# Kernel tuning notes

Hardware: AMD Instinct MI355X
Metric: run time of the kernel (lower is better)

## Reference

```python
import jax, jax.numpy as jnp
import numpy as np

B, T, E, A, S, H = 1024, 64, 1024, 10, 30, 200  # batch, time, embed, actdim, stoch, deter==hidden
MIN_STD = 0.1


def _xavier(key, fan_in, fan_out):
    lim = float(np.sqrt(6.0 / (fan_in + fan_out)))
    return jax.random.uniform(key, (fan_in, fan_out), jnp.float32, -lim, lim)


def setup_inputs() -> dict:
    key = jax.random.key(0)
    ks = jax.random.split(key, 20)
    gl = 1.0 / float(np.sqrt(H))  # torch GRUCell default init bound
    inp = {
        'embed': jax.random.normal(ks[0], (B, T, E), jnp.float32),
        'action': jax.random.normal(ks[1], (B, T, A), jnp.float32),
        'eps_post': jax.random.normal(ks[2], (T, B, S), jnp.float32),
        'eps_prior': jax.random.normal(ks[3], (T, B, S), jnp.float32),
        # Linear weights stored [in, out] (transposed vs torch) so x @ W works.
        'img1_w': _xavier(ks[4], A + S, H), 'img1_b': jnp.zeros((H,), jnp.float32),
        'gru_wi': jax.random.uniform(ks[5], (H, 3 * H), jnp.float32, -gl, gl),
        'gru_wh': jax.random.uniform(ks[6], (H, 3 * H), jnp.float32, -gl, gl),
        'gru_bi': jax.random.uniform(ks[7], (3 * H,), jnp.float32, -gl, gl),
        'gru_bh': jax.random.uniform(ks[8], (3 * H,), jnp.float32, -gl, gl),
        'img2_w': _xavier(ks[9], H, H), 'img2_b': jnp.zeros((H,), jnp.float32),
        'img3_w': _xavier(ks[10], H, 2 * S), 'img3_b': jnp.zeros((2 * S,), jnp.float32),
        'obs1_w': _xavier(ks[11], H + E, H), 'obs1_b': jnp.zeros((H,), jnp.float32),
        'obs2_w': _xavier(ks[12], H, 2 * S), 'obs2_b': jnp.zeros((2 * S,), jnp.float32),
    }
    return inp


def _observe(embed, action, eps_post, eps_prior,
             img1_w, img1_b, gru_wi, gru_wh, gru_bi, gru_bh,
             img2_w, img2_b, img3_w, img3_b, obs1_w, obs1_b, obs2_w, obs2_b):
    elu = jax.nn.elu
    embed_t = jnp.transpose(embed, (1, 0, 2))   # [T,B,E]
    action_t = jnp.transpose(action, (1, 0, 2))  # [T,B,A]

    def step(carry, xs):
        stoch, deter = carry
        a, emb, ep_q, ep_p = xs
        # img_step (prior)
        x = elu(jnp.concatenate([stoch, a], -1) @ img1_w + img1_b)
        gi = x @ gru_wi + gru_bi
        gh = deter @ gru_wh + gru_bh
        ir, iz, i_n = jnp.split(gi, 3, axis=-1)
        hr, hz, h_n = jnp.split(gh, 3, axis=-1)
        r = jax.nn.sigmoid(ir + hr)
        z = jax.nn.sigmoid(iz + hz)
        n = jnp.tanh(i_n + r * h_n)
        deter = (1.0 - z) * n + z * deter
        y = elu(deter @ img2_w + img2_b) @ img3_w + img3_b
        p_mean, p_std = jnp.split(y, 2, axis=-1)
        p_std = jax.nn.softplus(p_std) + MIN_STD
        p_stoch = p_mean + p_std * ep_p  # rsample
        # obs_step (posterior)
        o = elu(jnp.concatenate([deter, emb], -1) @ obs1_w + obs1_b) @ obs2_w + obs2_b
        q_mean, q_std = jnp.split(o, 2, axis=-1)
        q_std = jax.nn.softplus(q_std) + MIN_STD
        q_stoch = q_mean + q_std * ep_q  # rsample
        out = jnp.concatenate([q_mean, q_std, q_stoch, deter,
                               p_mean, p_std, p_stoch, deter], axis=-1)
        return (q_stoch, deter), out

    init = (jnp.zeros((B, S), embed.dtype), jnp.zeros((B, H), embed.dtype))
    _, outs = jax.lax.scan(step, init, (action_t, embed_t, eps_post, eps_prior))
    # outs: [T, B, 2*(3S+H)] -> [B, T, 580]; layout: post(mean,std,stoch,deter)|prior(mean,std,stoch,deter)
    return jnp.transpose(outs, (1, 0, 2))


def reference(embed, action, eps_post, eps_prior,
              img1_w, img1_b, gru_wi, gru_wh, gru_bi, gru_bh,
              img2_w, img2_b, img3_w, img3_b, obs1_w, obs1_b, obs2_w, obs2_b):
    return _observe(embed, action, eps_post, eps_prior,
                    img1_w, img1_b, gru_wi, gru_wh, gru_bi, gru_bh,
                    img2_w, img2_b, img3_w, img3_b, obs1_w, obs1_b, obs2_w, obs2_b)
```

## Files before the change

kernel.cpp:

```cpp
#include <hip/hip_runtime.h>

#define T_ 64

typedef __attribute__((ext_vector_type(4))) float f32x4;
typedef __attribute__((ext_vector_type(8))) short s16x8;

__device__ __forceinline__ unsigned short f2bf(float f) {
  unsigned u = __float_as_uint(f);
  u = (u + 0x7FFFu + ((u >> 16) & 1u)) >> 16;
  return (unsigned short)u;
}
__device__ __forceinline__ float bf2f(unsigned short h) {
  return __uint_as_float(((unsigned)h) << 16);
}
__device__ __forceinline__ float eluf(float x) { return x > 0.f ? x : __expf(x) - 1.f; }
__device__ __forceinline__ float sigmf(float x) { return 1.f / (1.f + __expf(-x)); }
__device__ __forceinline__ float tanh_(float x) {
  float xx = fminf(fmaxf(x, -30.f), 30.f);
  float e = __expf(-2.f * xx);
  return (1.f - e) / (1.f + e);
}
__device__ __forceinline__ float softpf(float x) {
  return x > 20.f ? x : __logf(1.f + __expf(x));
}

#define OPW1   0
#define OPWI   6656
#define OPWH   126464
#define OPO1D  246272
#define OPO2   286208
#define OPI2   298496
#define OPI3   345088
#define OWIWT  359424
#define OWHWT  364416
#define OO1DWT 369408
#define OI1WT  371072
#define OO2WT  372736
#define PK_U16 373248

#define OFF_PK  26214400
#define OFF_SWZ 26960896

__device__ void pack_mat(int idx, int stride, const float* __restrict__ W,
                         int K, int N, int KT, int NT, unsigned short* __restrict__ dst) {
  int total = KT * NT * 512;
  for (int i = idx; i < total; i += stride) {
    int j = i & 7, l = (i >> 3) & 63, rem = i >> 9;
    int kt = rem % KT, nt = rem / KT;
    int n = nt * 16 + (l & 15), k = kt * 32 + (l >> 4) * 8 + j;
    float v = (k < K && n < N) ? W[(size_t)k * N + n] : 0.f;
    dst[i] = f2bf(v);
  }
}

__device__ void pack_gate(int idx, int stride, const float* __restrict__ W,
                          unsigned short* __restrict__ dst) {
  int total = 3 * 13 * 6 * 512;
  for (int i = idx; i < total; i += stride) {
    int j = i & 7, l = (i >> 3) & 63, rem = i >> 9;
    int kt = rem % 6, rem2 = rem / 6, nt = rem2 % 13, g = rem2 / 13;
    int u = nt * 16 + (l & 15);
    int k = kt * 32 + (l >> 4) * 8 + j;
    float v = (u < 200) ? W[(size_t)k * 600 + g * 200 + u] : 0.f;
    dst[i] = f2bf(v);
  }
}

__global__ void prep_weights(const float* __restrict__ w1, const float* __restrict__ wi,
                             const float* __restrict__ wh, const float* __restrict__ i2,
                             const float* __restrict__ i3, const float* __restrict__ obs1w,
                             const float* __restrict__ o2,
                             unsigned short* __restrict__ pk,
                             unsigned short* __restrict__ swz) {
  int idx = blockIdx.x * blockDim.x + threadIdx.x;
  int stride = gridDim.x * blockDim.x;
  pack_mat(idx, stride, w1, 40, 200, 1, 13, pk + OPW1);
  pack_gate(idx, stride, wi, pk + OPWI);
  pack_gate(idx, stride, wh, pk + OPWH);
  pack_mat(idx, stride, obs1w, 200, 200, 6, 13, pk + OPO1D);
  pack_mat(idx, stride, o2, 200, 60, 6, 4, pk + OPO2);
  pack_mat(idx, stride, i2, 200, 200, 7, 13, pk + OPI2);
  pack_mat(idx, stride, i3, 200, 60, 7, 4, pk + OPI3);
  for (int i = idx; i < 4992; i += stride) {
    int j = i & 7, c = (i >> 3) % 208, g = i / 1664;
    pk[OWIWT + i] = f2bf((c < 200) ? wi[(size_t)(192 + j) * 600 + g * 200 + c] : 0.f);
    pk[OWHWT + i] = f2bf((c < 200) ? wh[(size_t)(192 + j) * 600 + g * 200 + c] : 0.f);
  }
  for (int i = idx; i < 1664; i += stride) {
    int c = i >> 3, j = i & 7;
    pk[OO1DWT + i] = f2bf((c < 200) ? obs1w[(size_t)(192 + j) * 200 + c] : 0.f);
    pk[OI1WT + i]  = f2bf((c < 200) ? w1[(size_t)(32 + j) * 200 + c] : 0.f);
  }
  for (int i = idx; i < 512; i += stride) {
    int c = i >> 3, j = i & 7;
    pk[OO2WT + i] = f2bf((c < 60) ? o2[(size_t)(192 + j) * 60 + c] : 0.f);
  }
  for (int i = idx; i < 212992; i += stride) {
    int j = i & 7, l = (i >> 3) & 63, rem = i >> 9;
    int nt = rem % 13, kc = rem / 13;
    int k = kc * 32 + ((l >> 4) * 8) + j;
    int n = nt * 16 + (l & 15);
    float v = (n < 200) ? obs1w[(size_t)(200 + k) * 200 + n] : 0.0f;
    swz[i] = f2bf(v);
  }
}

__global__ __launch_bounds__(256) void emb_gemm(const float* __restrict__ embed,
                                                const float* __restrict__ obs1b,
                                                const unsigned short* __restrict__ swz,
                                                unsigned short* __restrict__ emb_pre) {
  __shared__ __align__(16) unsigned short lds_A[64][40];
  int tid = threadIdx.x;
  int lane = tid & 63, w = tid >> 6;
  int R0 = blockIdx.x * 64;
  int tt = R0 >> 10;
  int bb = R0 & 1023;

  f32x4 acc[13];
#pragma unroll
  for (int nt = 0; nt < 13; ++nt) acc[nt] = (f32x4){0.f, 0.f, 0.f, 0.f};

  int i_row = tid >> 2, cg = tid & 3;
  const float* arow = embed + ((size_t)(bb + i_row) * 64 + tt) * 1024 + cg * 8;

  for (int kc = 0; kc < 32; ++kc) {
    __syncthreads();
    {
      const float* p = arow + kc * 32;
      f32x4 a0 = *(const f32x4*)p;
      f32x4 a1 = *(const f32x4*)(p + 4);
      unsigned short* dst = &lds_A[i_row][cg * 8];
      dst[0] = f2bf(a0[0]); dst[1] = f2bf(a0[1]); dst[2] = f2bf(a0[2]); dst[3] = f2bf(a0[3]);
      dst[4] = f2bf(a1[0]); dst[5] = f2bf(a1[1]); dst[6] = f2bf(a1[2]); dst[7] = f2bf(a1[3]);
    }
    __syncthreads();
    s16x8 af = *(const s16x8*)&lds_A[w * 16 + (lane & 15)][(lane >> 4) * 8];
    const unsigned short* bp = swz + (size_t)kc * 6656 + (size_t)lane * 8;
#pragma unroll
    for (int nt = 0; nt < 13; ++nt) {
      s16x8 bfv = *(const s16x8*)(bp + nt * 512);
      acc[nt] = __builtin_amdgcn_mfma_f32_16x16x32_bf16(af, bfv, acc[nt], 0, 0, 0);
    }
  }
  int r0 = R0 + w * 16 + ((lane >> 4) << 2);
  int c0 = lane & 15;
#pragma unroll
  for (int nt = 0; nt < 13; ++nt) {
    int n = nt * 16 + c0;
    if (n < 200) {
      float bv = obs1b[n];
#pragma unroll
      for (int rr = 0; rr < 4; ++rr)
        emb_pre[(size_t)(r0 + rr) * 200 + n] = f2bf(acc[nt][rr] + bv);
    }
  }
}

#define WAITVC(n) asm volatile("s_waitcnt vmcnt(" #n ")" ::: "memory")
#define LGKM0  asm volatile("s_waitcnt lgkmcnt(0)" ::: "memory")
#define MEMCLB asm volatile("" ::: "memory")
#define BAR()  __builtin_amdgcn_s_barrier()
#define SCHED0 __builtin_amdgcn_sched_barrier(0)
#define MFMA16(A, B, C) __builtin_amdgcn_mfma_f32_16x16x32_bf16((A), (B), (C), 0, 0, 0)

typedef __attribute__((address_space(3))) unsigned int u32_lds;
typedef const __attribute__((address_space(1))) unsigned int u32_glb;

__device__ __forceinline__ void gll16(const unsigned short* g, unsigned short* l, int lane) {
  __builtin_amdgcn_global_load_lds((u32_glb*)(g + lane * 8), (u32_lds*)l, 16, 0, 0);
}

__global__ __launch_bounds__(256, 1) void scan_v6(
    const float* __restrict__ action, const float* __restrict__ eps_post,
    const float* __restrict__ img1_b, const float* __restrict__ gru_bi,
    const float* __restrict__ gru_bh, const float* __restrict__ obs2_b,
    const unsigned short* __restrict__ pk, const unsigned short* __restrict__ emb_pre,
    float* __restrict__ out) {

  __shared__ __align__(16) unsigned short ring[4][12][512];
  __shared__ __align__(16) unsigned short l_w1[13 * 512];
  __shared__ __align__(16) unsigned short l_o2[24 * 512];
  __shared__ __align__(16) unsigned short l_wiWT[3][208][8];
  __shared__ __align__(16) unsigned short l_whWT[3][208][8];
  __shared__ __align__(16) unsigned short l_o1dWT[208][8];
  __shared__ __align__(16) unsigned short l_i1WT[208][8];
  __shared__ __align__(16) unsigned short l_o2WT[64][8];
  __shared__ __align__(16) unsigned short zblk[8];
  __shared__ __align__(16) unsigned short xoA[28][16][8];
  __shared__ __align__(16) unsigned short dA[28][16][8];
  __shared__ __align__(16) unsigned short sA[8][16][8];
  __shared__ __align__(16) float s_o[60][20];
  __shared__ __align__(16) float outbuf[16][292];
  __shared__ unsigned l_toff[4][96];

  const int tid = threadIdx.x, lane = tid & 63, w = tid >> 6;
  const int arow = lane & 15, kg = lane >> 4;
  const int b0 = blockIdx.x * 16;
  const int nug = (w == 0) ? 4 : 3;
  const int SW = nug * 24;
  unsigned short* ringw = &ring[w][0][0];

  for (int i = tid; i < 28 * 16 * 8; i += 256) { (&xoA[0][0][0])[i] = 0; (&dA[0][0][0])[i] = 0; }
  for (int i = tid; i < 8 * 16 * 8; i += 256) (&sA[0][0][0])[i] = 0;
  for (int i = tid; i < 13 * 512; i += 256) l_w1[i] = pk[OPW1 + i];
  for (int i = tid; i < 24 * 512; i += 256) l_o2[i] = pk[OPO2 + i];
  for (int i = tid; i < 4992; i += 256) (&l_wiWT[0][0][0])[i] = pk[OWIWT + i];
  for (int i = tid; i < 4992; i += 256) (&l_whWT[0][0][0])[i] = pk[OWHWT + i];
  for (int i = tid; i < 1664; i += 256) (&l_o1dWT[0][0])[i] = pk[OO1DWT + i];
  for (int i = tid; i < 1664; i += 256) (&l_i1WT[0][0])[i] = pk[OI1WT + i];
  for (int i = tid; i < 512; i += 256) (&l_o2WT[0][0])[i] = pk[OO2WT + i];
  if (tid < 8) zblk[tid] = 0;
  for (int i = tid; i < 4 * 96; i += 256) {
    int ww = i / 96, tau = i % 96;
    int iu = tau / 24, r2 = tau % 24, q = r2 / 6, kt = r2 % 6;
    int ug = ww + 4 * iu;
    unsigned off;
    if (q < 3) off = OPWI + (unsigned)((q * 13 + (ug <= 12 ? ug : 12)) * 6 + kt) * 512;
    else       off = OPWH + (unsigned)((2 * 13 + (ug <= 12 ? ug : 12)) * 6 + kt) * 512;
    l_toff[ww][tau] = off;
  }

  s16x8 wB[10][6];
#pragma unroll
  for (int s = 0; s < 10; ++s) {
    const unsigned short* base;
    if (w == 0) {
      if (s < 8) { int iu = s >> 1, g = s & 1; base = pk + OPWH + (size_t)((g * 13 + 4 * iu) * 6) * 512; }
      else if (s == 8) base = pk + OPO1D + (size_t)(12 * 6) * 512;
      else base = pk + OPO1D;
    } else {
      if (s < 6) { int iu = s >> 1, g = s & 1; base = pk + OPWH + (size_t)((g * 13 + (w + 4 * iu)) * 6) * 512; }
      else base = pk + OPO1D + (size_t)(((w - 1) + 3 * (s - 6)) * 6) * 512;
    }
#pragma unroll
    for (int kt = 0; kt < 6; ++kt)
      wB[s][kt] = *(const s16x8*)(base + (size_t)kt * 512 + lane * 8);
  }

  float bsum[4][2], bi2[4], bh2[4];
#pragma unroll
  for (int iu = 0; iu < 4; ++iu) {
    int u = (w + 4 * iu) * 16 + arow;
    bool vld = (iu < nug) && (u < 200);
    int uc = vld ? u : 0;
    float m = vld ? 1.f : 0.f;
    bsum[iu][0] = m * (gru_bi[uc] + gru_bh[uc]);
    bsum[iu][1] = m * (gru_bi[200 + uc] + gru_bh[200 + uc]);
    bi2[iu] = m * gru_bi[400 + uc];
    bh2[iu] = m * gru_bh[400 + uc];
  }
  float b1v[4];
#pragma unroll
  for (int i = 0; i < 4; ++i) {
    int nt = (i < 3) ? (w + 4 * i) : 12;
    int c = nt * 16 + arow;
    b1v[i] = (c < 200) ? img1_b[c] : 0.f;
  }
  float b5 = ((w * 16 + arow) < 60) ? obs2_b[w * 16 + arow] : 0.f;

  unsigned short e16[16];
#pragma unroll
  for (int i = 0; i < 4; ++i) {
    int nt4 = (w == 0) ? 12 : ((w - 1) + 3 * i);
    int c = nt4 * 16 + arow; int cc = (c < 200) ? c : 199;
#pragma unroll
    for (int rr = 0; rr < 4; ++rr)
      e16[i * 4 + rr] = emb_pre[((size_t)(b0 + kg * 4 + rr)) * 200 + cc];
  }
  float epsv[2];
  { int i1 = (tid + 256 < 480) ? tid + 256 : 479;
    epsv[0] = eps_post[((size_t)(b0 + tid / 30)) * 30 + tid % 30];
    epsv[1] = eps_post[((size_t)(b0 + i1 / 30)) * 30 + i1 % 30]; }
  float act0, actn;
  { int sl = (lane < 40) ? (w * 40 + lane) : (w * 40);
    act0 = action[((size_t)(b0 + sl / 10) * T_ + 0) * 10 + sl % 10];
    actn = action[((size_t)(b0 + sl / 10) * T_ + 1) * 10 + sl % 10]; }
  f32x4 dv[4];
#pragma unroll
  for (int iu = 0; iu < 4; ++iu) dv[iu] = (f32x4){0.f, 0.f, 0.f, 0.f};

  __syncthreads();
  if (lane < 40) {
    int sl = w * 40 + lane; int kk = sl % 10, r = sl / 10;
    sA[(30 + kk) >> 3][r][(30 + kk) & 7] = f2bf(act0);
  }
#pragma unroll
  for (int tt = 0; tt < 12; ++tt)
    gll16(pk + l_toff[w][tt], ringw + tt * 512, lane);
  WAITVC(0);
  __syncthreads();

  for (int t = 0; t < T_; ++t) {
    {
      s16x8 a0 = *(const s16x8*)&sA[kg][arow][0];
      s16x8 a1 = *(const s16x8*)&sA[4 + kg][arow][0];
#pragma unroll
      for (int i = 0; i < 4; ++i) {
        if (i < 3 || w == 0) {
          int nt = (i < 3) ? (w + 4 * i) : 12;
          int c = nt * 16 + arow;
          s16x8 B0 = *(const s16x8*)&l_w1[nt * 512 + lane * 8];
          f32x4 acc = {b1v[i], b1v[i], b1v[i], b1v[i]};
          acc = MFMA16(a0, B0, acc);
          s16x8 B1 = *(const s16x8*)((kg == 0) ? &l_i1WT[c][0] : &zblk[0]);
          acc = MFMA16(a1, B1, acc);
          if (c < 200) {
#pragma unroll
            for (int rr = 0; rr < 4; ++rr)
              xoA[c >> 3][kg * 4 + rr][c & 7] = f2bf(eluf(acc[rr]));
          }
        }
      }
    }
    LGKM0; BAR();

    {
#pragma unroll
      for (int iu = 0; iu < 4; ++iu) {
        if (iu < 3 || w == 0) {
          const int uu = (w + 4 * iu) * 16 + arow;
          const int uuc = (uu < 208) ? uu : 207;
          s16x8 ax[6], ad[6];
#pragma unroll
          for (int kt = 0; kt < 6; ++kt) {
            ax[kt] = *(const s16x8*)&xoA[kt * 4 + kg][arow][0];
            ad[kt] = *(const s16x8*)&dA[kt * 4 + kg][arow][0];
          }
          s16x8 ax6 = *(const s16x8*)&xoA[24 + kg][arow][0];
          s16x8 ad6 = *(const s16x8*)&dA[24 + kg][arow][0];
          f32x4 gv[2], gin, ghn;
#pragma unroll
          for (int q = 0; q < 4; ++q) {
            const int beta = iu * 4 + q;
            if (beta < 2) { WAITVC(30); } else { WAITVC(6); }
            float b = (q < 2) ? bsum[iu][q & 1] : ((q == 2) ? bi2[iu] : bh2[iu]);
            f32x4 acc = {b, b, b, b};
#pragma unroll
            for (int kt = 0; kt < 6; ++kt) {
              const int slot = (beta * 6 + kt) % 12;
              s16x8 Bv = *(const s16x8*)(ringw + slot * 512 + lane * 8);
              acc = MFMA16((q == 3) ? ad[kt] : ax[kt], Bv, acc);
            }
            MEMCLB; SCHED0;
#pragma unroll
            for (int k2 = 0; k2 < 6; ++k2) {
              const int ttc = beta * 6 + 12 + k2;
              int tm = (ttc >= SW) ? ttc - SW : ttc;
              gll16(pk + l_toff[w][tm], ringw + ((ttc % 12) * 512), lane);
            }
            if (q < 2) {
              { const unsigned short* wp = (kg == 0) ? &l_wiWT[q][uuc][0] : &zblk[0];
                acc = MFMA16(ax6, *(const s16x8*)wp, acc); }
              const int s_ = iu * 2 + q;
#pragma unroll
              for (int kt = 0; kt < 6; ++kt) acc = MFMA16(ad[kt], wB[s_][kt], acc);
              { const unsigned short* wp = (kg == 0) ? &l_whWT[q][uuc][0] : &zblk[0];
                acc = MFMA16(ad6, *(const s16x8*)wp, acc); }
              gv[q] = acc;
            } else if (q == 2) {
              const unsigned short* wp = (kg == 0) ? &l_wiWT[2][uuc][0] : &zblk[0];
              gin = MFMA16(ax6, *(const s16x8*)wp, acc);
            } else {
              const unsigned short* wp = (kg == 0) ? &l_whWT[2][uuc][0] : &zblk[0];
              ghn = MFMA16(ad6, *(const s16x8*)wp, acc);
            }
          }
#pragma unroll
          for (int rr = 0; rr < 4; ++rr) {
            float r = sigmf(gv[0][rr]);
            float z = sigmf(gv[1][rr]);
            float n = tanh_(gin[rr] + r * ghn[rr]);
            dv[iu][rr] = (1.f - z) * n + z * dv[iu][rr];
          }
          if (uu < 200) {
#pragma unroll
            for (int rr = 0; rr < 4; ++rr) outbuf[kg * 4 + rr][90 + uu] = dv[iu][rr];
          }
        }
      }
    }
    LGKM0; BAR();

#pragma unroll
    for (int iu = 0; iu < 4; ++iu) {
      if (iu < 3 || w == 0) {
        int uu = (w + 4 * iu) * 16 + arow;
        if (uu < 200) {
#pragma unroll
          for (int rr = 0; rr < 4; ++rr)
            dA[uu >> 3][kg * 4 + rr][uu & 7] = f2bf(dv[iu][rr]);
        }
      }
    }
    LGKM0; BAR();

    {
      s16x8 ad4[6];
#pragma unroll
      for (int kt = 0; kt < 6; ++kt) ad4[kt] = *(const s16x8*)&dA[kt * 4 + kg][arow][0];
      s16x8 ad46 = *(const s16x8*)&dA[24 + kg][arow][0];
      if (w == 0) {
        int c = 192 + arow;
        f32x4 acc = {0.f, 0.f, 0.f, 0.f};
#pragma unroll
        for (int kt = 0; kt < 6; ++kt) acc = MFMA16(ad4[kt], wB[8][kt], acc);
        { const unsigned short* wp = (kg == 0) ? &l_o1dWT[c][0] : &zblk[0];
          acc = MFMA16(ad46, *(const s16x8*)wp, acc); }
        if (c < 200) {
#pragma unroll
          for (int rr = 0; rr < 4; ++rr)
            xoA[c >> 3][kg * 4 + rr][c & 7] = f2bf(eluf(acc[rr] + bf2f(e16[rr])));
        }
      } else {
#pragma unroll
        for (int i = 0; i < 4; ++i) {
          int c = ((w - 1) + 3 * i) * 16 + arow;
          f32x4 acc = {0.f, 0.f, 0.f, 0.f};
#pragma unroll
          for (int kt = 0; kt < 6; ++kt) acc = MFMA16(ad4[kt], wB[6 + i][kt], acc);
          { const unsigned short* wp = (kg == 0) ? &l_o1dWT[c][0] : &zblk[0];
            acc = MFMA16(ad46, *(const s16x8*)wp, acc); }
#pragma unroll
          for (int rr = 0; rr < 4; ++rr)
            xoA[c >> 3][kg * 4 + rr][c & 7] = f2bf(eluf(acc[rr] + bf2f(e16[i * 4 + rr])));
        }
      }
    }
    LGKM0; BAR();

    {
      s16x8 a5[6];
#pragma unroll
      for (int kt = 0; kt < 6; ++kt) a5[kt] = *(const s16x8*)&xoA[kt * 4 + kg][arow][0];
      s16x8 a56 = *(const s16x8*)&xoA[24 + kg][arow][0];
      int c5 = w * 16 + arow;
      f32x4 acc = {b5, b5, b5, b5};
#pragma unroll
      for (int kt = 0; kt < 6; ++kt) {
        s16x8 Bv = *(const s16x8*)&l_o2[(w * 6 + kt) * 512 + lane * 8];
        acc = MFMA16(a5[kt], Bv, acc);
      }
      { const unsigned short* wp = (kg == 0) ? &l_o2WT[c5][0] : &zblk[0];
        acc = MFMA16(a56, *(const s16x8*)wp, acc); }
      if (c5 < 60) *(f32x4*)&s_o[c5][kg * 4] = acc;
    }
    LGKM0; BAR();

    {
#pragma unroll
      for (int rep = 0; rep < 2; ++rep) {
        int it = tid + rep * 256;
        bool v = it < 480;
        int itc = v ? it : 479;
        int r = itc / 30, j = itc % 30;
        float qm = s_o[j][r];
        float qs = softpf(s_o[j + 30][r]) + 0.1f;
        float qst = qm + qs * epsv[rep];
        if (v) {
          outbuf[r][j] = qm; outbuf[r][30 + j] = qs; outbuf[r][60 + j] = qst;
          sA[j >> 3][r][j & 7] = f2bf(qst);
        }
      }
      if (lane < 40) {
        int sl = w * 40 + lane; int kk = sl % 10, r = sl / 10;
        sA[(30 + kk) >> 3][r][(30 + kk) & 7] = f2bf(actn);
      }
      int tc = (t + 1 < T_) ? t + 1 : T_ - 1;
      int ta = (t + 2 < T_) ? t + 2 : T_ - 1;
#pragma unroll
      for (int i = 0; i < 4; ++i) {
        int nt4 = (w == 0) ? 12 : ((w - 1) + 3 * i);
        int c = nt4 * 16 + arow; int cc = (c < 200) ? c : 199;
#pragma unroll
        for (int rr = 0; rr < 4; ++rr)
          e16[i * 4 + rr] = emb_pre[((size_t)tc * 1024 + b0 + kg * 4 + rr) * 200 + cc];
      }
      { int i1 = (tid + 256 < 480) ? tid + 256 : 479;
        epsv[0] = eps_post[((size_t)tc * 1024 + b0 + tid / 30) * 30 + tid % 30];
        epsv[1] = eps_post[((size_t)tc * 1024 + b0 + i1 / 30) * 30 + i1 % 30]; }
      { int sl = (lane < 40) ? (w * 40 + lane) : (w * 40);
        actn = action[((size_t)(b0 + sl / 10) * T_ + ta) * 10 + sl % 10]; }
    }
    LGKM0; BAR();

#pragma unroll
    for (int k2 = 0; k2 < 5; ++k2) {
      int idx = tid + k2 * 256; idx = (idx < 1168) ? idx : 1167;
      int row = idx / 73, ci = idx - row * 73;
      f32x4 v = *(const f32x4*)&outbuf[row][ci * 4];
      *(f32x4*)(out + ((size_t)(b0 + row) * T_ + t) * 580 + ci * 4) = v;
    }
  }
}

__global__ __launch_bounds__(256) void post_head(const float* __restrict__ eps_prior,
                                                 const float* __restrict__ img2_b,
                                                 const float* __restrict__ img3_b,
                                                 const unsigned short* __restrict__ pk,
                                                 float* __restrict__ out) {
  __shared__ __align__(16) unsigned short dAp[4][28][16][8];
  __shared__ __align__(16) unsigned short y1p[4][28][16][8];
  __shared__ __align__(16) float s_p[60][68];
  int b = blockIdx.x;
  int tid = threadIdx.x;
  int lane = tid & 63, w = tid >> 6, arow = lane & 15, kg = lane >> 4;

  for (int i = tid; i < 1536; i += 256) {
    int mt = i / 384, rem = i % 384;
    int gidx = 25 + rem / 128, r2 = (rem % 128) / 8, j = rem & 7;
    dAp[mt][gidx][r2][j] = 0;
    y1p[mt][gidx][r2][j] = 0;
  }
  for (int i = tid; i < 12800; i += 256) {
    int row = i / 200, c = i % 200;
    float v = out[((size_t)(b * 64 + row)) * 580 + 90 + c];
    dAp[row >> 4][c >> 3][row & 15][c & 7] = f2bf(v);
  }
  __syncthreads();

  s16x8 ad[7];
#pragma unroll
  for (int kt = 0; kt < 7; ++kt) ad[kt] = *(const s16x8*)&dAp[w][kt * 4 + kg][arow][0];
#pragma unroll
  for (int nt = 0; nt < 13; ++nt) {
    int col = nt * 16 + arow;
    float bv = (col < 200) ? img2_b[col] : 0.f;
    f32x4 acc = {bv, bv, bv, bv};
#pragma unroll
    for (int kt = 0; kt < 7; ++kt) {
      s16x8 Bv = *(const s16x8*)(pk + OPI2 + (size_t)((nt * 7 + kt) * 512) + lane * 8);
      acc = __builtin_amdgcn_mfma_f32_16x16x32_bf16(ad[kt], Bv, acc, 0, 0, 0);
    }
    if (col < 200) {
#pragma unroll
      for (int rr = 0; rr < 4; ++rr)
        y1p[w][col >> 3][kg * 4 + rr][col & 7] = f2bf(eluf(acc[rr]));
    }
  }
  __syncthreads();

  s16x8 ay[7];
#pragma unroll
  for (int kt = 0; kt < 7; ++kt) ay[kt] = *(const s16x8*)&y1p[w][kt * 4 + kg][arow][0];
#pragma unroll
  for (int nt = 0; nt < 4; ++nt) {
    int col = nt * 16 + arow;
    float bv = (col < 60) ? img3_b[col] : 0.f;
    f32x4 acc = {bv, bv, bv, bv};
#pragma unroll
    for (int kt = 0; kt < 7; ++kt) {
      s16x8 Bv = *(const s16x8*)(pk + OPI3 + (size_t)((nt * 7 + kt) * 512) + lane * 8);
      acc = __builtin_amdgcn_mfma_f32_16x16x32_bf16(ay[kt], Bv, acc, 0, 0, 0);
    }
    if (col < 60) {
#pragma unroll
      for (int rr = 0; rr < 4; ++rr) s_p[col][w * 16 + kg * 4 + rr] = acc[rr];
    }
  }
  __syncthreads();

  for (int i = tid; i < 1920; i += 256) {
    int row = i / 30, j = i % 30;
    float pm = s_p[j][row];
    float ps = softpf(s_p[j + 30][row]) + 0.1f;
    float pst = pm + ps * eps_prior[((size_t)row * 1024 + b) * 30 + j];
    size_t ob = ((size_t)b * 64 + row) * 580;
    out[ob + 290 + j] = pm;
    out[ob + 320 + j] = ps;
    out[ob + 350 + j] = pst;
  }
  for (int i = tid; i < 6400; i += 256) {
    int row = i / 100, c2 = i % 100;
    size_t ob = ((size_t)b * 64 + row) * 580;
    *(float2*)&out[ob + 380 + c2 * 2] = *(const float2*)&out[ob + 90 + c2 * 2];
  }
}

extern "C" void kernel_launch(void* const* d_in, const int* in_sizes, int n_in,
                              void* d_out, int out_size, void* d_ws, size_t ws_size,
                              hipStream_t stream) {
  const float* embed    = (const float*)d_in[0];
  const float* action   = (const float*)d_in[1];
  const float* eps_post = (const float*)d_in[2];
  const float* eps_prior= (const float*)d_in[3];
  const float* img1_w   = (const float*)d_in[4];
  const float* img1_b   = (const float*)d_in[5];
  const float* gru_wi   = (const float*)d_in[6];
  const float* gru_wh   = (const float*)d_in[7];
  const float* gru_bi   = (const float*)d_in[8];
  const float* gru_bh   = (const float*)d_in[9];
  const float* img2_w   = (const float*)d_in[10];
  const float* img2_b   = (const float*)d_in[11];
  const float* img3_w   = (const float*)d_in[12];
  const float* img3_b   = (const float*)d_in[13];
  const float* obs1_w   = (const float*)d_in[14];
  const float* obs1_b   = (const float*)d_in[15];
  const float* obs2_w   = (const float*)d_in[16];
  const float* obs2_b   = (const float*)d_in[17];

  char* ws = (char*)d_ws;
  unsigned short* emb_pre = (unsigned short*)ws;
  unsigned short* pkw     = (unsigned short*)(ws + OFF_PK);
  unsigned short* swz     = (unsigned short*)(ws + OFF_SWZ);
  float* outp = (float*)d_out;

  prep_weights<<<256, 256, 0, stream>>>(img1_w, gru_wi, gru_wh, img2_w, img3_w,
                                        obs1_w, obs2_w, pkw, swz);
  emb_gemm<<<1024, 256, 0, stream>>>(embed, obs1_b, swz, emb_pre);
  scan_v6<<<64, 256, 0, stream>>>(action, eps_post, img1_b, gru_bi, gru_bh,
                                  obs2_b, pkw, emb_pre, outp);
  post_head<<<1024, 256, 0, stream>>>(eps_prior, img2_b, img3_b, pkw, outp);
}
```

Measured before the change: 996.2 us.

## Process 32 batch rows per scan block, reusing each weight fragment for two MFMAs

The recurrent scan kernel now handles 32 batch rows per block instead of 16, launching 32 blocks instead of 64, so each streamed or register-resident weight fragment feeds two MFMA tiles. The weight streaming ring is reorganized into a double-buffered issue/consume scheme with templated wait counts, and the output staging buffer is replaced by direct nontemporal global stores. This halves per-row weight traffic per step but uses only half the CUs and adds register pressure, which risks a longer serial chain per block.

```diff
diff --git a/kernel.cpp b/kernel.cpp
--- a/kernel.cpp
+++ b/kernel.cpp
@@ -156,12 +156,13 @@
   }
 }
 
-#define WAITVC(n) asm volatile("s_waitcnt vmcnt(" #n ")" ::: "memory")
 #define LGKM0  asm volatile("s_waitcnt lgkmcnt(0)" ::: "memory")
 #define MEMCLB asm volatile("" ::: "memory")
 #define BAR()  __builtin_amdgcn_s_barrier()
-#define SCHED0 __builtin_amdgcn_sched_barrier(0)
 #define MFMA16(A, B, C) __builtin_amdgcn_mfma_f32_16x16x32_bf16((A), (B), (C), 0, 0, 0)
+#define WV12 asm volatile("s_waitcnt vmcnt(12)" ::: "memory")
+#define WV6  asm volatile("s_waitcnt vmcnt(6)" ::: "memory")
+#define WV0  asm volatile("s_waitcnt vmcnt(0)" ::: "memory")
 
 typedef __attribute__((address_space(3))) unsigned int u32_lds;
 typedef const __attribute__((address_space(1))) unsigned int u32_glb;
@@ -170,7 +171,70 @@
   __builtin_amdgcn_global_load_lds((u32_glb*)(g + lane * 8), (u32_lds*)l, 16, 0, 0);
 }
 
-__global__ __launch_bounds__(256, 1) void scan_v6(
+__device__ __forceinline__ unsigned taddr(int w, int g, int kt) {
+  if (g >= 16) return OPO1D + (unsigned)((12 * 6 + kt) * 512);
+  if (g >= 12 && w != 0) {
+    int nt = (w - 1) + 3 * (g - 12);
+    return OPO1D + (unsigned)((nt * 6 + kt) * 512);
+  }
+  int iu = g >> 2, q = g & 3;
+  int ug = w + 4 * iu;
+  return (q < 3) ? OPWI + (unsigned)(((q * 13 + ug) * 6 + kt) * 512)
+                 : OPWH + (unsigned)(((2 * 13 + ug) * 6 + kt) * 512);
+}
+
+__device__ __forceinline__ void issue6(int g, unsigned short* ringw,
+                                       const unsigned short* pk, int w, int lane) {
+#pragma unroll
+  for (int kt = 0; kt < 6; ++kt)
+    gll16(pk + taddr(w, g, kt), ringw + (((g & 1) * 6 + kt) * 512), lane);
+}
+
+template <int B, bool LAST, bool ISSUE>
+__device__ __forceinline__ void consq(const s16x8* A0, const s16x8* A1,
+                                      f32x4& ca, f32x4& cb, unsigned short* ringw,
+                                      const unsigned short* pk, int w, int lane) {
+  if (LAST) { WV0; } else { WV6; }
+#pragma unroll
+  for (int kt = 0; kt < 6; ++kt) {
+    s16x8 Bv = *(const s16x8*)(ringw + (((B & 1) * 6 + kt) * 512) + lane * 8);
+    ca = MFMA16(A0[kt], Bv, ca);
+    cb = MFMA16(A1[kt], Bv, cb);
+  }
+  if (ISSUE) {
+    LGKM0; MEMCLB;
+    issue6(B + 2, ringw, pk, w, lane);
+    MEMCLB;
+  }
+}
+
+__device__ __forceinline__ void res6p(const s16x8* A0, const s16x8* A1,
+                                      const s16x8* Wt, f32x4& ca, f32x4& cb) {
+#pragma unroll
+  for (int kt = 0; kt < 6; ++kt) {
+    ca = MFMA16(A0[kt], Wt[kt], ca);
+    cb = MFMA16(A1[kt], Wt[kt], cb);
+  }
+}
+__device__ __forceinline__ void rem1p(const s16x8& A60, const s16x8& A61,
+                                      const unsigned short* wt, const unsigned short* zb,
+                                      bool kg0, f32x4& ca, f32x4& cb) {
+  s16x8 W = *(const s16x8*)(kg0 ? wt : zb);
+  ca = MFMA16(A60, W, ca);
+  cb = MFMA16(A61, W, cb);
+}
+__device__ __forceinline__ void grustep(const f32x4& rv, const f32x4& zv,
+                                        const f32x4& inv, const f32x4& hnv, f32x4& dv) {
+#pragma unroll
+  for (int rr = 0; rr < 4; ++rr) {
+    float r = sigmf(rv[rr]);
+    float z = sigmf(zv[rr]);
+    float n = tanh_(inv[rr] + r * hnv[rr]);
+    dv[rr] = (1.f - z) * n + z * dv[rr];
+  }
+}
+
+__global__ __launch_bounds__(256, 1) void scan_v12(
     const float* __restrict__ action, const float* __restrict__ eps_post,
     const float* __restrict__ img1_b, const float* __restrict__ gru_bi,
     const float* __restrict__ gru_bh, const float* __restrict__ obs2_b,
@@ -186,128 +250,137 @@
   __shared__ __align__(16) unsigned short l_i1WT[208][8];
   __shared__ __align__(16) unsigned short l_o2WT[64][8];
   __shared__ __align__(16) unsigned short zblk[8];
-  __shared__ __align__(16) unsigned short xoA[28][16][8];
-  __shared__ __align__(16) unsigned short dA[28][16][8];
-  __shared__ __align__(16) unsigned short sA[8][16][8];
-  __shared__ __align__(16) float s_o[60][20];
-  __shared__ __align__(16) float outbuf[16][292];
-  __shared__ unsigned l_toff[4][96];
+  __shared__ __align__(16) unsigned short xoA[28][32][8];
+  __shared__ __align__(16) unsigned short dA[28][32][8];
+  __shared__ __align__(16) unsigned short sA[8][32][8];
+  __shared__ __align__(16) float s_o[60][36];
 
   const int tid = threadIdx.x, lane = tid & 63, w = tid >> 6;
   const int arow = lane & 15, kg = lane >> 4;
-  const int b0 = blockIdx.x * 16;
-  const int nug = (w == 0) ? 4 : 3;
-  const int SW = nug * 24;
+  const bool kg0 = (kg == 0);
+  const int b0 = blockIdx.x * 32;
   unsigned short* ringw = &ring[w][0][0];
 
-  for (int i = tid; i < 28 * 16 * 8; i += 256) { (&xoA[0][0][0])[i] = 0; (&dA[0][0][0])[i] = 0; }
-  for (int i = tid; i < 8 * 16 * 8; i += 256) (&sA[0][0][0])[i] = 0;
+  for (int i = tid; i < 7168; i += 256) { (&xoA[0][0][0])[i] = 0; (&dA[0][0][0])[i] = 0; }
+  for (int i = tid; i < 2048; i += 256) (&sA[0][0][0])[i] = 0;
   for (int i = tid; i < 13 * 512; i += 256) l_w1[i] = pk[OPW1 + i];
   for (int i = tid; i < 24 * 512; i += 256) l_o2[i] = pk[OPO2 + i];
-  for (int i = tid; i < 4992; i += 256) (&l_wiWT[0][0][0])[i] = pk[OWIWT + i];
-  for (int i = tid; i < 4992; i += 256) (&l_whWT[0][0][0])[i] = pk[OWHWT + i];
-  for (int i = tid; i < 1664; i += 256) (&l_o1dWT[0][0])[i] = pk[OO1DWT + i];
-  for (int i = tid; i < 1664; i += 256) (&l_i1WT[0][0])[i] = pk[OI1WT + i];
+  for (int i = tid; i < 4992; i += 256) {
+    (&l_wiWT[0][0][0])[i] = pk[OWIWT + i];
+    (&l_whWT[0][0][0])[i] = pk[OWHWT + i];
+  }
+  for (int i = tid; i < 1664; i += 256) {
+    (&l_o1dWT[0][0])[i] = pk[OO1DWT + i];
+    (&l_i1WT[0][0])[i] = pk[OI1WT + i];
+  }
   for (int i = tid; i < 512; i += 256) (&l_o2WT[0][0])[i] = pk[OO2WT + i];
   if (tid < 8) zblk[tid] = 0;
-  for (int i = tid; i < 4 * 96; i += 256) {
-    int ww = i / 96, tau = i % 96;
-    int iu = tau / 24, r2 = tau % 24, q = r2 / 6, kt = r2 % 6;
-    int ug = ww + 4 * iu;
-    unsigned off;
-    if (q < 3) off = OPWI + (unsigned)((q * 13 + (ug <= 12 ? ug : 12)) * 6 + kt) * 512;
-    else       off = OPWH + (unsigned)((2 * 13 + (ug <= 12 ? ug : 12)) * 6 + kt) * 512;
-    l_toff[ww][tau] = off;
-  }
-
-  s16x8 wB[10][6];
-#pragma unroll
-  for (int s = 0; s < 10; ++s) {
-    const unsigned short* base;
-    if (w == 0) {
-      if (s < 8) { int iu = s >> 1, g = s & 1; base = pk + OPWH + (size_t)((g * 13 + 4 * iu) * 6) * 512; }
-      else if (s == 8) base = pk + OPO1D + (size_t)(12 * 6) * 512;
-      else base = pk + OPO1D;
-    } else {
-      if (s < 6) { int iu = s >> 1, g = s & 1; base = pk + OPWH + (size_t)((g * 13 + (w + 4 * iu)) * 6) * 512; }
-      else base = pk + OPO1D + (size_t)(((w - 1) + 3 * (s - 6)) * 6) * 512;
-    }
+
+  const int nug = (w == 0) ? 4 : 3;
+  s16x8 wB[8][6];
+#pragma unroll
+  for (int s = 0; s < 8; ++s) {
+    int iu = s >> 1, g = s & 1;
+    int ug = (iu < nug) ? (w + 4 * iu) : w;
+    const unsigned short* base = pk + OPWH + (size_t)((g * 13 + ug) * 6) * 512;
 #pragma unroll
     for (int kt = 0; kt < 6; ++kt)
       wB[s][kt] = *(const s16x8*)(base + (size_t)kt * 512 + lane * 8);
   }
 
-  float bsum[4][2], bi2[4], bh2[4];
+  float bs0[4], bs1[4], bi2v[4], bh2v[4], b1v[4];
+  int uWT[4];
 #pragma unroll
   for (int iu = 0; iu < 4; ++iu) {
-    int u = (w + 4 * iu) * 16 + arow;
-    bool vld = (iu < nug) && (u < 200);
-    int uc = vld ? u : 0;
-    float m = vld ? 1.f : 0.f;
-    bsum[iu][0] = m * (gru_bi[uc] + gru_bh[uc]);
-    bsum[iu][1] = m * (gru_bi[200 + uc] + gru_bh[200 + uc]);
-    bi2[iu] = m * gru_bi[400 + uc];
-    bh2[iu] = m * gru_bh[400 + uc];
-  }
-  float b1v[4];
+    bool vld = (iu < 3 || w == 0);
+    int ug = w + 4 * iu;
+    int u = ug * 16 + arow;
+    uWT[iu] = vld ? u : 0;
+    bool m = vld && (u < 200);
+    int uc = m ? u : 0;
+    float mm = m ? 1.f : 0.f;
+    bs0[iu] = mm * (gru_bi[uc] + gru_bh[uc]);
+    bs1[iu] = mm * (gru_bi[200 + uc] + gru_bh[200 + uc]);
+    bi2v[iu] = mm * gru_bi[400 + uc];
+    bh2v[iu] = mm * gru_bh[400 + uc];
+    b1v[iu] = mm * img1_b[uc];
+  }
+  const int c5 = w * 16 + arow;
+  const float b5 = (c5 < 60) ? obs2_b[c5] : 0.f;
+
+  unsigned short e16[32];
+#pragma unroll
+  for (int i = 0; i < 32; ++i) e16[i] = 0;
 #pragma unroll
   for (int i = 0; i < 4; ++i) {
-    int nt = (i < 3) ? (w + 4 * i) : 12;
-    int c = nt * 16 + arow;
-    b1v[i] = (c < 200) ? img1_b[c] : 0.f;
-  }
-  float b5 = ((w * 16 + arow) < 60) ? obs2_b[w * 16 + arow] : 0.f;
-
-  unsigned short e16[16];
-#pragma unroll
-  for (int i = 0; i < 4; ++i) {
-    int nt4 = (w == 0) ? 12 : ((w - 1) + 3 * i);
-    int c = nt4 * 16 + arow; int cc = (c < 200) ? c : 199;
-#pragma unroll
-    for (int rr = 0; rr < 4; ++rr)
-      e16[i * 4 + rr] = emb_pre[((size_t)(b0 + kg * 4 + rr)) * 200 + cc];
-  }
-  float epsv[2];
-  { int i1 = (tid + 256 < 480) ? tid + 256 : 479;
-    epsv[0] = eps_post[((size_t)(b0 + tid / 30)) * 30 + tid % 30];
-    epsv[1] = eps_post[((size_t)(b0 + i1 / 30)) * 30 + i1 % 30]; }
-  float act0, actn;
-  { int sl = (lane < 40) ? (w * 40 + lane) : (w * 40);
-    act0 = action[((size_t)(b0 + sl / 10) * T_ + 0) * 10 + sl % 10];
-    actn = action[((size_t)(b0 + sl / 10) * T_ + 1) * 10 + sl % 10]; }
-  f32x4 dv[4];
-#pragma unroll
-  for (int iu = 0; iu < 4; ++iu) dv[iu] = (f32x4){0.f, 0.f, 0.f, 0.f};
+    if (i == 0 || w != 0) {
+      int nt = (w == 0) ? 12 : ((w - 1) + 3 * i);
+      int c = nt * 16 + arow;
+      int cc = (c < 200) ? c : 199;
+#pragma unroll
+      for (int h = 0; h < 2; ++h)
+#pragma unroll
+        for (int rr = 0; rr < 4; ++rr)
+          e16[i * 8 + h * 4 + rr] = __builtin_nontemporal_load(
+              &emb_pre[((size_t)(b0 + h * 16 + kg * 4 + rr)) * 200 + cc]);
+    }
+  }
+  float epsv[4];
+#pragma unroll
+  for (int k2 = 0; k2 < 4; ++k2) {
+    int idx = tid + k2 * 256; idx = (idx < 960) ? idx : 959;
+    epsv[k2] = __builtin_nontemporal_load(&eps_post[((size_t)(b0 + idx / 30)) * 30 + idx % 30]);
+  }
+  float act0[2], actn[2];
+#pragma unroll
+  for (int k2 = 0; k2 < 2; ++k2) {
+    int sl = tid + k2 * 256; sl = (sl < 320) ? sl : 319;
+    act0[k2] = __builtin_nontemporal_load(&action[((size_t)(b0 + sl / 10) * T_ + 0) * 10 + sl % 10]);
+    actn[k2] = __builtin_nontemporal_load(&action[((size_t)(b0 + sl / 10) * T_ + 1) * 10 + sl % 10]);
+  }
+  f32x4 dv[4][2];
+#pragma unroll
+  for (int iu = 0; iu < 4; ++iu)
+#pragma unroll
+    for (int h = 0; h < 2; ++h) dv[iu][h] = (f32x4){0.f, 0.f, 0.f, 0.f};
 
   __syncthreads();
-  if (lane < 40) {
-    int sl = w * 40 + lane; int kk = sl % 10, r = sl / 10;
-    sA[(30 + kk) >> 3][r][(30 + kk) & 7] = f2bf(act0);
-  }
-#pragma unroll
-  for (int tt = 0; tt < 12; ++tt)
-    gll16(pk + l_toff[w][tt], ringw + tt * 512, lane);
-  WAITVC(0);
+#pragma unroll
+  for (int k2 = 0; k2 < 2; ++k2) {
+    int sl = tid + k2 * 256;
+    if (sl < 320) {
+      int r = sl / 10, kk = sl % 10;
+      sA[(30 + kk) >> 3][r][(30 + kk) & 7] = f2bf(act0[k2]);
+    }
+  }
+  issue6(0, ringw, pk, w, lane);
+  issue6(1, ringw, pk, w, lane);
+  WV0;
   __syncthreads();
 
   for (int t = 0; t < T_; ++t) {
     {
-      s16x8 a0 = *(const s16x8*)&sA[kg][arow][0];
-      s16x8 a1 = *(const s16x8*)&sA[4 + kg][arow][0];
-#pragma unroll
-      for (int i = 0; i < 4; ++i) {
-        if (i < 3 || w == 0) {
-          int nt = (i < 3) ? (w + 4 * i) : 12;
+      s16x8 a00 = *(const s16x8*)&sA[kg][arow][0];
+      s16x8 a01 = *(const s16x8*)&sA[kg][16 + arow][0];
+      s16x8 a10 = *(const s16x8*)&sA[4 + kg][arow][0];
+      s16x8 a11 = *(const s16x8*)&sA[4 + kg][16 + arow][0];
+#pragma unroll
+      for (int iu = 0; iu < 4; ++iu) {
+        if (iu < 3 || w == 0) {
+          int nt = (iu < 3) ? (w + 4 * iu) : 12;
           int c = nt * 16 + arow;
           s16x8 B0 = *(const s16x8*)&l_w1[nt * 512 + lane * 8];
-          f32x4 acc = {b1v[i], b1v[i], b1v[i], b1v[i]};
-          acc = MFMA16(a0, B0, acc);
-          s16x8 B1 = *(const s16x8*)((kg == 0) ? &l_i1WT[c][0] : &zblk[0]);
-          acc = MFMA16(a1, B1, acc);
+          f32x4 xa = {b1v[iu], b1v[iu], b1v[iu], b1v[iu]};
+          f32x4 xb = xa;
+          xa = MFMA16(a00, B0, xa);
+          xb = MFMA16(a01, B0, xb);
+          rem1p(a10, a11, &l_i1WT[c][0], zblk, kg0, xa, xb);
           if (c < 200) {
 #pragma unroll
-            for (int rr = 0; rr < 4; ++rr)
-              xoA[c >> 3][kg * 4 + rr][c & 7] = f2bf(eluf(acc[rr]));
+            for (int rr = 0; rr < 4; ++rr) {
+              xoA[c >> 3][kg * 4 + rr][c & 7] = f2bf(eluf(xa[rr]));
+              xoA[c >> 3][16 + kg * 4 + rr][c & 7] = f2bf(eluf(xb[rr]));
+            }
           }
         }
       }
@@ -315,181 +388,208 @@
     LGKM0; BAR();
 
     {
-#pragma unroll
-      for (int iu = 0; iu < 4; ++iu) {
-        if (iu < 3 || w == 0) {
-          const int uu = (w + 4 * iu) * 16 + arow;
-          const int uuc = (uu < 208) ? uu : 207;
-          s16x8 ax[6], ad[6];
-#pragma unroll
-          for (int kt = 0; kt < 6; ++kt) {
-            ax[kt] = *(const s16x8*)&xoA[kt * 4 + kg][arow][0];
-            ad[kt] = *(const s16x8*)&dA[kt * 4 + kg][arow][0];
-          }
-          s16x8 ax6 = *(const s16x8*)&xoA[24 + kg][arow][0];
-          s16x8 ad6 = *(const s16x8*)&dA[24 + kg][arow][0];
-          f32x4 gv[2], gin, ghn;
-#pragma unroll
-          for (int q = 0; q < 4; ++q) {
-            const int beta = iu * 4 + q;
-            if (beta < 2) { WAITVC(30); } else { WAITVC(6); }
-            float b = (q < 2) ? bsum[iu][q & 1] : ((q == 2) ? bi2[iu] : bh2[iu]);
-            f32x4 acc = {b, b, b, b};
-#pragma unroll
-            for (int kt = 0; kt < 6; ++kt) {
-              const int slot = (beta * 6 + kt) % 12;
-              s16x8 Bv = *(const s16x8*)(ringw + slot * 512 + lane * 8);
-              acc = MFMA16((q == 3) ? ad[kt] : ax[kt], Bv, acc);
-            }
-            MEMCLB; SCHED0;
-#pragma unroll
-            for (int k2 = 0; k2 < 6; ++k2) {
-              const int ttc = beta * 6 + 12 + k2;
-              int tm = (ttc >= SW) ? ttc - SW : ttc;
-              gll16(pk + l_toff[w][tm], ringw + ((ttc % 12) * 512), lane);
-            }
-            if (q < 2) {
-              { const unsigned short* wp = (kg == 0) ? &l_wiWT[q][uuc][0] : &zblk[0];
-                acc = MFMA16(ax6, *(const s16x8*)wp, acc); }
-              const int s_ = iu * 2 + q;
-#pragma unroll
-              for (int kt = 0; kt < 6; ++kt) acc = MFMA16(ad[kt], wB[s_][kt], acc);
-              { const unsigned short* wp = (kg == 0) ? &l_whWT[q][uuc][0] : &zblk[0];
-                acc = MFMA16(ad6, *(const s16x8*)wp, acc); }
-              gv[q] = acc;
-            } else if (q == 2) {
-              const unsigned short* wp = (kg == 0) ? &l_wiWT[2][uuc][0] : &zblk[0];
-              gin = MFMA16(ax6, *(const s16x8*)wp, acc);
-            } else {
-              const unsigned short* wp = (kg == 0) ? &l_whWT[2][uuc][0] : &zblk[0];
-              ghn = MFMA16(ad6, *(const s16x8*)wp, acc);
-            }
-          }
+      s16x8 ax0[6], ax1[6], ad0[6], ad1[6];
+#pragma unroll
+      for (int kt = 0; kt < 6; ++kt) {
+        ax0[kt] = *(const s16x8*)&xoA[kt * 4 + kg][arow][0];
+        ax1[kt] = *(const s16x8*)&xoA[kt * 4 + kg][16 + arow][0];
+        ad0[kt] = *(const s16x8*)&dA[kt * 4 + kg][arow][0];
+        ad1[kt] = *(const s16x8*)&dA[kt * 4 + kg][16 + arow][0];
+      }
+      s16x8 ax60 = *(const s16x8*)&xoA[24 + kg][arow][0];
+      s16x8 ax61 = *(const s16x8*)&xoA[24 + kg][16 + arow][0];
+      s16x8 ad60 = *(const s16x8*)&dA[24 + kg][arow][0];
+      s16x8 ad61 = *(const s16x8*)&dA[24 + kg][16 + arow][0];
+
+#define UG_BODY(IU, LQ3)                                                          \
+      {                                                                           \
+        const int uc = uWT[IU];                                                   \
+        f32x4 rva = {bs0[IU], bs0[IU], bs0[IU], bs0[IU]}, rvb = rva;              \
+        consq<IU * 4 + 0, false, true>(ax0, ax1, rva, rvb, ringw, pk, w, lane);   \
+        rem1p(ax60, ax61, &l_wiWT[0][uc][0], zblk, kg0, rva, rvb);                \
+        res6p(ad0, ad1, wB[IU * 2 + 0], rva, rvb);                                \
+        rem1p(ad60, ad61, &l_whWT[0][uc][0], zblk, kg0, rva, rvb);                \
+        f32x4 zva = {bs1[IU], bs1[IU], bs1[IU], bs1[IU]}, zvb = zva;              \
+        consq<IU * 4 + 1, false, true>(ax0, ax1, zva, zvb, ringw, pk, w, lane);   \
+        rem1p(ax60, ax61, &l_wiWT[1][uc][0], zblk, kg0, zva, zvb);                \
+        res6p(ad0, ad1, wB[IU * 2 + 1], zva, zvb);                                \
+        rem1p(ad60, ad61, &l_whWT[1][uc][0], zblk, kg0, zva, zvb);                \
+        f32x4 iva = {bi2v[IU], bi2v[IU], bi2v[IU], bi2v[IU]}, ivb = iva;          \
+        consq<IU * 4 + 2, false, true>(ax0, ax1, iva, ivb, ringw, pk, w, lane);   \
+        rem1p(ax60, ax61, &l_wiWT[2][uc][0], zblk, kg0, iva, ivb);                \
+        f32x4 hva = {bh2v[IU], bh2v[IU], bh2v[IU], bh2v[IU]}, hvb = hva;          \
+        consq<IU * 4 + 3, false, LQ3>(ad0, ad1, hva, hvb, ringw, pk, w, lane);    \
+        rem1p(ad60, ad61, &l_whWT[2][uc][0], zblk, kg0, hva, hvb);                \
+        grustep(rva, zva, iva, hva, dv[IU][0]);                                   \
+        grustep(rvb, zvb, ivb, hvb, dv[IU][1]);                                   \
+      }
+      UG_BODY(0, true)
+      UG_BODY(1, true)
+      UG_BODY(2, true)
+      if (w == 0) { UG_BODY(3, false) }
+#undef UG_BODY
+    }
+    LGKM0; BAR();
+
+#pragma unroll
+    for (int iu = 0; iu < 4; ++iu) {
+      if (iu < 3 || w == 0) {
+        int u = (w + 4 * iu) * 16 + arow;
+        if (u < 200) {
 #pragma unroll
           for (int rr = 0; rr < 4; ++rr) {
-            float r = sigmf(gv[0][rr]);
-            float z = sigmf(gv[1][rr]);
-            float n = tanh_(gin[rr] + r * ghn[rr]);
-            dv[iu][rr] = (1.f - z) * n + z * dv[iu][rr];
-          }
-          if (uu < 200) {
-#pragma unroll
-            for (int rr = 0; rr < 4; ++rr) outbuf[kg * 4 + rr][90 + uu] = dv[iu][rr];
+            dA[u >> 3][kg * 4 + rr][u & 7] = f2bf(dv[iu][0][rr]);
+            dA[u >> 3][16 + kg * 4 + rr][u & 7] = f2bf(dv[iu][1][rr]);
           }
         }
       }
     }
     LGKM0; BAR();
 
+    {
+      s16x8 ad40[6], ad41[6];
+#pragma unroll
+      for (int kt = 0; kt < 6; ++kt) {
+        ad40[kt] = *(const s16x8*)&dA[kt * 4 + kg][arow][0];
+        ad41[kt] = *(const s16x8*)&dA[kt * 4 + kg][16 + arow][0];
+      }
+      s16x8 ad460 = *(const s16x8*)&dA[24 + kg][arow][0];
+      s16x8 ad461 = *(const s16x8*)&dA[24 + kg][16 + arow][0];
+      if (w != 0) {
+#define O1_BODY(I, LST, ISS)                                                      \
+        {                                                                         \
+          int c = ((w - 1) + 3 * (I)) * 16 + arow;                                \
+          f32x4 oa = {0.f, 0.f, 0.f, 0.f}, ob = oa;                               \
+          consq<12 + (I), LST, ISS>(ad40, ad41, oa, ob, ringw, pk, w, lane);      \
+          rem1p(ad460, ad461, &l_o1dWT[c][0], zblk, kg0, oa, ob);                 \
+          for (int rr = 0; rr < 4; ++rr) {                                        \
+            xoA[c >> 3][kg * 4 + rr][c & 7] =                                     \
+                f2bf(eluf(oa[rr] + bf2f(e16[(I) * 8 + rr])));                     \
+            xoA[c >> 3][16 + kg * 4 + rr][c & 7] =                                \
+                f2bf(eluf(ob[rr] + bf2f(e16[(I) * 8 + 4 + rr])));                 \
+          }                                                                       \
+        }
+        O1_BODY(0, false, true)
+        O1_BODY(1, false, true)
+        O1_BODY(2, false, false)
+        O1_BODY(3, true, false)
+#undef O1_BODY
+      } else {
+        int c = 192 + arow;
+        f32x4 oa = {0.f, 0.f, 0.f, 0.f}, ob = oa;
+        consq<16, true, false>(ad40, ad41, oa, ob, ringw, pk, w, lane);
+        rem1p(ad460, ad461, &l_o1dWT[c][0], zblk, kg0, oa, ob);
+        if (c < 200) {
+#pragma unroll
+          for (int rr = 0; rr < 4; ++rr) {
+            xoA[c >> 3][kg * 4 + rr][c & 7] = f2bf(eluf(oa[rr] + bf2f(e16[rr])));
+            xoA[c >> 3][16 + kg * 4 + rr][c & 7] = f2bf(eluf(ob[rr] + bf2f(e16[4 + rr])));
+          }
+        }
+      }
+    }
+    LGKM0; BAR();
+
+    {
+      s16x8 a50[6], a51[6];
+#pragma unroll
+      for (int kt = 0; kt < 6; ++kt) {
+        a50[kt] = *(const s16x8*)&xoA[kt * 4 + kg][arow][0];
+        a51[kt] = *(const s16x8*)&xoA[kt * 4 + kg][16 + arow][0];
+      }
+      s16x8 a560 = *(const s16x8*)&xoA[24 + kg][arow][0];
+      s16x8 a561 = *(const s16x8*)&xoA[24 + kg][16 + arow][0];
+      f32x4 pa = {b5, b5, b5, b5}, pb = pa;
+#pragma unroll
+      for (int kt = 0; kt < 6; ++kt) {
+        s16x8 Bv = *(const s16x8*)&l_o2[(w * 6 + kt) * 512 + lane * 8];
+        pa = MFMA16(a50[kt], Bv, pa);
+        pb = MFMA16(a51[kt], Bv, pb);
+      }
+      rem1p(a560, a561, &l_o2WT[c5][0], zblk, kg0, pa, pb);
+      if (c5 < 60) {
+        *(f32x4*)&s_o[c5][kg * 4] = pa;
+        *(f32x4*)&s_o[c5][16 + kg * 4] = pb;
+      }
+    }
+    LGKM0; BAR();
+
+    {
+#pragma unroll
+      for (int k2 = 0; k2 < 4; ++k2) {
+        int idx = tid + k2 * 256;
+        bool v = idx < 960;
+        int ic = v ? idx : 959;
+        int r = ic / 30, j = ic % 30;
+        float qm = s_o[j][r];
+        float qs = softpf(s_o[j + 30][r]) + 0.1f;
+        float qst = qm + qs * epsv[k2];
+        size_t ob = ((size_t)(b0 + r) * T_ + t) * 580;
+        if (v) {
+          __builtin_nontemporal_store(qm, out + ob + j);
+          __builtin_nontemporal_store(qs, out + ob + 30 + j);
+          __builtin_nontemporal_store(qst, out + ob + 60 + j);
+          sA[j >> 3][r][j & 7] = f2bf(qst);
+        }
+      }
+#pragma unroll
+      for (int k2 = 0; k2 < 2; ++k2) {
+        int sl = tid + k2 * 256;
+        if (sl < 320) {
+          int r = sl / 10, kk = sl % 10;
+          sA[(30 + kk) >> 3][r][(30 + kk) & 7] = f2bf(actn[k2]);
+        }
+      }
+      int tc = (t + 1 < T_) ? t + 1 : T_ - 1;
+      int ta = (t + 2 < T_) ? t + 2 : T_ - 1;
+#pragma unroll
+      for (int i = 0; i < 4; ++i) {
+        if (i == 0 || w != 0) {
+          int nt = (w == 0) ? 12 : ((w - 1) + 3 * i);
+          int c = nt * 16 + arow;
+          int cc = (c < 200) ? c : 199;
+#pragma unroll
+          for (int h = 0; h < 2; ++h)
+#pragma unroll
+            for (int rr = 0; rr < 4; ++rr)
+              e16[i * 8 + h * 4 + rr] = __builtin_nontemporal_load(
+                  &emb_pre[((size_t)tc * 1024 + b0 + h * 16 + kg * 4 + rr) * 200 + cc]);
+        }
+      }
+#pragma unroll
+      for (int k2 = 0; k2 < 4; ++k2) {
+        int idx = tid + k2 * 256; idx = (idx < 960) ? idx : 959;
+        epsv[k2] = __builtin_nontemporal_load(
+            &eps_post[((size_t)tc * 1024 + b0 + idx / 30) * 30 + idx % 30]);
+      }
+#pragma unroll
+      for (int k2 = 0; k2 < 2; ++k2) {
+        int sl = tid + k2 * 256; sl = (sl < 320) ? sl : 319;
+        actn[k2] = __builtin_nontemporal_load(
+            &action[((size_t)(b0 + sl / 10) * T_ + ta) * 10 + sl % 10]);
+      }
+    }
+    LGKM0; BAR();
+
 #pragma unroll
     for (int iu = 0; iu < 4; ++iu) {
       if (iu < 3 || w == 0) {
-        int uu = (w + 4 * iu) * 16 + arow;
-        if (uu < 200) {
-#pragma unroll
-          for (int rr = 0; rr < 4; ++rr)
-            dA[uu >> 3][kg * 4 + rr][uu & 7] = f2bf(dv[iu][rr]);
+        int u = (w + 4 * iu) * 16 + arow;
+        if (u < 200) {
+#pragma unroll
+          for (int h = 0; h < 2; ++h)
+#pragma unroll
+            for (int rr = 0; rr < 4; ++rr)
+              __builtin_nontemporal_store(dv[iu][h][rr],
+                  out + ((size_t)(b0 + h * 16 + kg * 4 + rr) * T_ + t) * 580 + 90 + u);
         }
       }
     }
-    LGKM0; BAR();
-
-    {
-      s16x8 ad4[6];
-#pragma unroll
-      for (int kt = 0; kt < 6; ++kt) ad4[kt] = *(const s16x8*)&dA[kt * 4 + kg][arow][0];
-      s16x8 ad46 = *(const s16x8*)&dA[24 + kg][arow][0];
-      if (w == 0) {
-        int c = 192 + arow;
-        f32x4 acc = {0.f, 0.f, 0.f, 0.f};
-#pragma unroll
-        for (int kt = 0; kt < 6; ++kt) acc = MFMA16(ad4[kt], wB[8][kt], acc);
-        { const unsigned short* wp = (kg == 0) ? &l_o1dWT[c][0] : &zblk[0];
-          acc = MFMA16(ad46, *(const s16x8*)wp, acc); }
-        if (c < 200) {
-#pragma unroll
-          for (int rr = 0; rr < 4; ++rr)
-            xoA[c >> 3][kg * 4 + rr][c & 7] = f2bf(eluf(acc[rr] + bf2f(e16[rr])));
-        }
-      } else {
-#pragma unroll
-        for (int i = 0; i < 4; ++i) {
-          int c = ((w - 1) + 3 * i) * 16 + arow;
-          f32x4 acc = {0.f, 0.f, 0.f, 0.f};
-#pragma unroll
-          for (int kt = 0; kt < 6; ++kt) acc = MFMA16(ad4[kt], wB[6 + i][kt], acc);
-          { const unsigned short* wp = (kg == 0) ? &l_o1dWT[c][0] : &zblk[0];
-            acc = MFMA16(ad46, *(const s16x8*)wp, acc); }
-#pragma unroll
-          for (int rr = 0; rr < 4; ++rr)
-            xoA[c >> 3][kg * 4 + rr][c & 7] = f2bf(eluf(acc[rr] + bf2f(e16[i * 4 + rr])));
-        }
-      }
-    }
-    LGKM0; BAR();
-
-    {
-      s16x8 a5[6];
-#pragma unroll
-      for (int kt = 0; kt < 6; ++kt) a5[kt] = *(const s16x8*)&xoA[kt * 4 + kg][arow][0];
-      s16x8 a56 = *(const s16x8*)&xoA[24 + kg][arow][0];
-      int c5 = w * 16 + arow;
-      f32x4 acc = {b5, b5, b5, b5};
-#pragma unroll
-      for (int kt = 0; kt < 6; ++kt) {
-        s16x8 Bv = *(const s16x8*)&l_o2[(w * 6 + kt) * 512 + lane * 8];
-        acc = MFMA16(a5[kt], Bv, acc);
-      }
-      { const unsigned short* wp = (kg == 0) ? &l_o2WT[c5][0] : &zblk[0];
-        acc = MFMA16(a56, *(const s16x8*)wp, acc); }
-      if (c5 < 60) *(f32x4*)&s_o[c5][kg * 4] = acc;
-    }
-    LGKM0; BAR();
-
-    {
-#pragma unroll
-      for (int rep = 0; rep < 2; ++rep) {
-        int it = tid + rep * 256;
-        bool v = it < 480;
-        int itc = v ? it : 479;
-        int r = itc / 30, j = itc % 30;
-        float qm = s_o[j][r];
-        float qs = softpf(s_o[j + 30][r]) + 0.1f;
-        float qst = qm + qs * epsv[rep];
-        if (v) {
-          outbuf[r][j] = qm; outbuf[r][30 + j] = qs; outbuf[r][60 + j] = qst;
-          sA[j >> 3][r][j & 7] = f2bf(qst);
-        }
-      }
-      if (lane < 40) {
-        int sl = w * 40 + lane; int kk = sl % 10, r = sl / 10;
-        sA[(30 + kk) >> 3][r][(30 + kk) & 7] = f2bf(actn);
-      }
-      int tc = (t + 1 < T_) ? t + 1 : T_ - 1;
-      int ta = (t + 2 < T_) ? t + 2 : T_ - 1;
-#pragma unroll
-      for (int i = 0; i < 4; ++i) {
-        int nt4 = (w == 0) ? 12 : ((w - 1) + 3 * i);
-        int c = nt4 * 16 + arow; int cc = (c < 200) ? c : 199;
-#pragma unroll
-        for (int rr = 0; rr < 4; ++rr)
-          e16[i * 4 + rr] = emb_pre[((size_t)tc * 1024 + b0 + kg * 4 + rr) * 200 + cc];
-      }
-      { int i1 = (tid + 256 < 480) ? tid + 256 : 479;
-        epsv[0] = eps_post[((size_t)tc * 1024 + b0 + tid / 30) * 30 + tid % 30];
-        epsv[1] = eps_post[((size_t)tc * 1024 + b0 + i1 / 30) * 30 + i1 % 30]; }
-      { int sl = (lane < 40) ? (w * 40 + lane) : (w * 40);
-        actn = action[((size_t)(b0 + sl / 10) * T_ + ta) * 10 + sl % 10]; }
-    }
-    LGKM0; BAR();
-
-#pragma unroll
-    for (int k2 = 0; k2 < 5; ++k2) {
-      int idx = tid + k2 * 256; idx = (idx < 1168) ? idx : 1167;
-      int row = idx / 73, ci = idx - row * 73;
-      f32x4 v = *(const f32x4*)&outbuf[row][ci * 4];
-      *(f32x4*)(out + ((size_t)(b0 + row) * T_ + t) * 580 + ci * 4) = v;
-    }
+    MEMCLB;
+    issue6(0, ringw, pk, w, lane);
+    issue6(1, ringw, pk, w, lane);
+    WV12;
+    MEMCLB;
   }
 }
 
@@ -607,7 +707,7 @@
   prep_weights<<<256, 256, 0, stream>>>(img1_w, gru_wi, gru_wh, img2_w, img3_w,
                                         obs1_w, obs2_w, pkw, swz);
   emb_gemm<<<1024, 256, 0, stream>>>(embed, obs1_b, swz, emb_pre);
-  scan_v6<<<64, 256, 0, stream>>>(action, eps_post, img1_b, gru_bi, gru_bh,
-                                  obs2_b, pkw, emb_pre, outp);
+  scan_v12<<<32, 256, 0, stream>>>(action, eps_post, img1_b, gru_bi, gru_bh,
+                                   obs2_b, pkw, emb_pre, outp);
   post_head<<<1024, 256, 0, stream>>>(eps_prior, img2_b, img3_b, pkw, outp);
 }
```

Result: slower. 2.857 ms (+186.8%).
